# Performance work log

Measured on AMD Instinct MI355X. Metric: run time of the kernel, lower is better.

Reference implementation:

```python
import jax, jax.numpy as jnp
import numpy as np

W_DIST = 1.0
W_ANGLE = 1.0
EPS = 1e-12


def setup_inputs() -> dict:
    key = jax.random.key(0)
    k1, k2, k3 = jax.random.split(key, 3)
    B, C = 384, 512
    return {
        "feat_s": jax.random.normal(k1, (B, C), dtype=jnp.float32),
        "feat_t": jax.random.normal(k2, (B, C), dtype=jnp.float32),
        "labels": jax.random.randint(k3, (B,), 0, C, dtype=jnp.int64),
    }


def _pdist(feat):
    # Euclidean pairwise distances with zeroed diagonal (matches RKD.pdist).
    sq = jnp.sum(feat * feat, axis=1)                      # [B]
    prod = feat @ feat.T                                   # [B,B]
    d = jnp.clip(sq[None, :] + sq[:, None] - 2.0 * prod, EPS, None)
    d = jnp.sqrt(d)
    B = feat.shape[0]
    return d * (1.0 - jnp.eye(B, dtype=feat.dtype))


def _norm_pdist(feat):
    d = _pdist(feat)
    pos = d > 0
    mean_pos = jnp.sum(jnp.where(pos, d, 0.0)) / jnp.maximum(jnp.sum(pos), 1)
    return d / mean_pos


def _smooth_l1(x, y):
    a = jnp.abs(x - y)
    return jnp.mean(jnp.where(a < 1.0, 0.5 * a * a, a - 0.5))


def _angle_gram(feat):
    # vd[i, j] = feat[j] - feat[i], normalized along feature dim (F.normalize eps=1e-12)
    vd = feat[None, :, :] - feat[:, None, :]               # [B,B,C]
    nrm = jnp.sqrt(jnp.sum(vd * vd, axis=2, keepdims=True))
    vd = vd / jnp.maximum(nrm, EPS)
    return jnp.einsum('bic,bjc->bij', vd, vd)              # [B,B,B]


def _rkd(feat_s, feat_t):
    dist_loss = _smooth_l1(_norm_pdist(feat_s), _norm_pdist(feat_t))
    angle_loss = _smooth_l1(_angle_gram(feat_s), _angle_gram(feat_t))
    return W_DIST * dist_loss + W_ANGLE * angle_loss


def reference(feat_s, feat_t, labels):
    # hard CE loss (mean reduction)
    logp = jax.nn.log_softmax(feat_s, axis=-1)
    hard_loss = -jnp.mean(logp[jnp.arange(feat_s.shape[0]), labels])
    # soft RKD loss; teacher detached as in the torch code
    soft_loss = _rkd(feat_s, jax.lax.stop_gradient(feat_t))
    return hard_loss + soft_loss
```

## Files before the change

kernel.cpp:

```cpp
#include <hip/hip_runtime.h>
#include <hip/hip_bf16.h>
#include <math.h>

#define B 384
#define C 512
#define NPAIR (B * B)
#define NOFF  (B * (B - 1))

#define T16  24
#define UP16 300
#define T64  6
#define UP64 21

#define HARD_OFF 0
#define DSUM_OFF 384
#define ANG_OFF  984
#define DIST_OFF 1992
#define SQS_OFF  2016
#define SQT_OFF  2400
#define PS_OFF   2816
#define PT_OFF   (PS_OFF + NPAIR)

typedef __attribute__((ext_vector_type(8))) short short8;
typedef __attribute__((ext_vector_type(4))) float floatx4;

__device__ __forceinline__ float blk_sum(float v, float* s4, int t) {
#pragma unroll
  for (int off = 32; off > 0; off >>= 1) v += __shfl_down(v, off, 64);
  if ((t & 63) == 0) s4[t >> 6] = v;
  __syncthreads();
  float r = s4[0] + s4[1] + s4[2] + s4[3];
  __syncthreads();
  return r;
}

__device__ __forceinline__ short bfc(float x) {
  __hip_bfloat16 h = __float2bfloat16(x);
  return __builtin_bit_cast(short, h);
}

__device__ __forceinline__ short8 load_frag(const float* p) {
  float4 lo = *(const float4*)p;
  float4 hi = *(const float4*)(p + 4);
  short8 v;
  v[0] = bfc(lo.x); v[1] = bfc(lo.y); v[2] = bfc(lo.z); v[3] = bfc(lo.w);
  v[4] = bfc(hi.x); v[5] = bfc(hi.y); v[6] = bfc(hi.z); v[7] = bfc(hi.w);
  return v;
}

__global__ __launch_bounds__(256) void k_row(const float* __restrict__ fs,
                                             const float* __restrict__ ft,
                                             const int* __restrict__ lab,
                                             float* __restrict__ ws) {
  int r = blockIdx.x, t = threadIdx.x;
  const float* xs = fs + r * C;
  const float* xt = ft + r * C;
  float x0 = xs[t], x1 = xs[t + 256];
  float y0 = xt[t], y1 = xt[t + 256];
  __shared__ float s4[4];
  float m = fmaxf(x0, x1);
#pragma unroll
  for (int off = 32; off > 0; off >>= 1) m = fmaxf(m, __shfl_down(m, off, 64));
  if ((t & 63) == 0) s4[t >> 6] = m;
  __syncthreads();
  m = fmaxf(fmaxf(s4[0], s4[1]), fmaxf(s4[2], s4[3]));
  __syncthreads();
  float es = blk_sum(expf(x0 - m) + expf(x1 - m), s4, t);
  float ss = blk_sum(x0 * x0 + x1 * x1, s4, t);
  float st = blk_sum(y0 * y0 + y1 * y1, s4, t);
  if (t == 0) {
    ws[SQS_OFF + r] = ss;
    ws[SQT_OFF + r] = st;
    ws[HARD_OFF + r] = m + logf(es) - xs[lab[r]];
  }
}

__global__ __launch_bounds__(256, 4) void k_gram(const float* __restrict__ fs,
                                                 const float* __restrict__ ft,
                                                 float* __restrict__ ws) {
  int t = threadIdx.x;
  int w = t >> 6, lane = t & 63;
  int g = blockIdx.x * 4 + w;
  int tensor = (g >= UP16) ? 1 : 0;
  int uu = g - tensor * UP16;
  int ti = 0;
  while (uu >= T16 - ti) { uu -= T16 - ti; ++ti; }
  int tj = ti + uu;
  const float* F = tensor ? ft : fs;
  const float* sq = ws + (tensor ? SQT_OFF : SQS_OFF);
  float* P = ws + (tensor ? PT_OFF : PS_OFF);
  int i0 = ti * 16, j0 = tj * 16;
  int r = lane & 15, q = lane >> 4;
  const float* arow = F + (i0 + r) * C + q * 8;
  const float* brow = F + (j0 + r) * C + q * 8;
  floatx4 acc = {0.f, 0.f, 0.f, 0.f};
#pragma unroll
  for (int ks = 0; ks < 16; ++ks) {
    short8 a = load_frag(arow + ks * 32);
    short8 b = load_frag(brow + ks * 32);
    acc = __builtin_amdgcn_mfma_f32_16x16x32_bf16(a, b, acc, 0, 0, 0);
  }
  int col = lane & 15;
  int j = j0 + col;
  float sqj = sq[j];
  float dsum = 0.f;
#pragma unroll
  for (int reg = 0; reg < 4; ++reg) {
    int i = i0 + q * 4 + reg;
    float p = acc[reg];
    P[i * B + j] = p;
    P[j * B + i] = p;
    float d2 = sq[i] + sqj - 2.f * p;
    float d = sqrtf(fmaxf(d2, 1e-12f));
    float wgt = (ti < tj) ? 2.f : ((i < j) ? 2.f : 0.f);
    dsum = fmaf(wgt, d, dsum);
  }
#pragma unroll
  for (int off = 32; off > 0; off >>= 1) dsum += __shfl_down(dsum, off, 64);
  if (lane == 0) ws[DSUM_OFF + g] = dsum;
}

#define BCH 8
#define ANGLE_BODY(MASKED)                                                   \
  for (int b = 0; b < BCH; ++b) {                                            \
    float uis[4], qis[4], uit[4], qit[4], ujs[4], qjs[4], ujt[4], qjt[4];    \
    float4 v;                                                                \
    v = *(const float4*)&sI[b][0][ty * 4];                                   \
    uis[0] = v.x; uis[1] = v.y; uis[2] = v.z; uis[3] = v.w;                  \
    v = *(const float4*)&sI[b][1][ty * 4];                                   \
    qis[0] = v.x; qis[1] = v.y; qis[2] = v.z; qis[3] = v.w;                  \
    v = *(const float4*)&sI[b][2][ty * 4];                                   \
    uit[0] = v.x; uit[1] = v.y; uit[2] = v.z; uit[3] = v.w;                  \
    v = *(const float4*)&sI[b][3][ty * 4];                                   \
    qit[0] = v.x; qit[1] = v.y; qit[2] = v.z; qit[3] = v.w;                  \
    v = *(const float4*)&sJ[b][0][tx * 4];                                   \
    ujs[0] = v.x; ujs[1] = v.y; ujs[2] = v.z; ujs[3] = v.w;                  \
    v = *(const float4*)&sJ[b][1][tx * 4];                                   \
    qjs[0] = v.x; qjs[1] = v.y; qjs[2] = v.z; qjs[3] = v.w;                  \
    v = *(const float4*)&sJ[b][2][tx * 4];                                   \
    ujt[0] = v.x; ujt[1] = v.y; ujt[2] = v.z; ujt[3] = v.w;                  \
    v = *(const float4*)&sJ[b][3][tx * 4];                                   \
    qjt[0] = v.x; qjt[1] = v.y; qjt[2] = v.z; qjt[3] = v.w;                  \
    _Pragma("unroll")                                                        \
    for (int r = 0; r < 4; ++r) {                                            \
      _Pragma("unroll")                                                      \
      for (int c = 0; c < 4; ++c) {                                          \
        float f1s = fmaf(uis[r], ps[r][c], -qis[r]);                         \
        float gs = fmaf(ujs[c], f1s, -(uis[r] * qjs[c]));                    \
        float f1t = fmaf(uit[r], pt[r][c], -qit[r]);                         \
        float gt = fmaf(ujt[c], f1t, -(uit[r] * qjt[c]));                    \
        float a = fabsf(gs - gt);                                            \
        if (MASKED) a = (ty * 4 + r < tx * 4 + c) ? a : 0.f;                 \
        float mm = fminf(a, 1.f);                                            \
        acc = fmaf(mm, fmaf(-0.5f, mm, a), acc);                             \
      }                                                                      \
    }                                                                        \
  }

__global__ __launch_bounds__(256, 4) void k_angle(float* __restrict__ ws) {
  const float* Ps = ws + PS_OFF;
  const float* Pt = ws + PT_OFF;
  const float* sqs = ws + SQS_OFF;
  const float* sqt = ws + SQT_OFF;
  int uu = blockIdx.x;
  int ti = 0;
  while (uu >= T64 - ti) { uu -= T64 - ti; ++ti; }
  int tj = ti + uu;
  int i0 = ti * 64, j0 = tj * 64;
  bool diag = (ti == tj);
  int b0 = blockIdx.y * BCH;
  int t = threadIdx.x;
  int ty = t >> 4, tx = t & 15;

  __shared__ float sI[BCH][4][64];
  __shared__ float sJ[BCH][4][64];
  __shared__ float s4[4];

  float ps[4][4], pt[4][4];
#pragma unroll
  for (int r = 0; r < 4; ++r) {
    float4 v = *(const float4*)&Ps[(i0 + ty * 4 + r) * B + j0 + tx * 4];
    ps[r][0] = v.x; ps[r][1] = v.y; ps[r][2] = v.z; ps[r][3] = v.w;
    v = *(const float4*)&Pt[(i0 + ty * 4 + r) * B + j0 + tx * 4];
    pt[r][0] = v.x; pt[r][1] = v.y; pt[r][2] = v.z; pt[r][3] = v.w;
  }

  for (int idx = t; idx < BCH * 128; idx += 256) {
    int b = idx >> 7, p = idx & 127;
    int bb = b0 + b;
    int col = (p < 64) ? (i0 + p) : (j0 + p - 64);
    float pvs = Ps[bb * B + col];
    float pvt = Pt[bb * B + col];
    float pbbs = Ps[bb * B + bb];
    float pbbt = Pt[bb * B + bb];
    float d2s = sqs[bb] + sqs[col] - 2.f * pvs;
    float d2t = sqt[bb] + sqt[col] - 2.f * pvt;
    float us = (col == bb) ? 0.f : rsqrtf(fmaxf(d2s, 1e-24f));
    float ut = (col == bb) ? 0.f : rsqrtf(fmaxf(d2t, 1e-24f));
    float qs = us * (pvs - 0.5f * pbbs);
    float qt = ut * (pvt - 0.5f * pbbt);
    float* dst = (p < 64) ? &sI[b][0][p] : &sJ[b][0][p - 64];
    dst[0] = us; dst[64] = qs; dst[128] = ut; dst[192] = qt;
  }
  __syncthreads();

  float acc = 0.f;
  if (diag) { ANGLE_BODY(true) } else { ANGLE_BODY(false) }

  float asum = blk_sum(acc, s4, t);
  if (t == 0) ws[ANG_OFF + blockIdx.y * UP64 + blockIdx.x] = asum;

  if (blockIdx.y == 0) {
    float ssum = 0.f, tsum = 0.f;
    for (int i = t; i < UP16; i += 256) ssum += ws[DSUM_OFF + i];
    for (int i = t; i < UP16; i += 256) tsum += ws[DSUM_OFF + UP16 + i];
    ssum = blk_sum(ssum, s4, t);
    tsum = blk_sum(tsum, s4, t);
    float inv_ms = (float)NOFF / ssum;
    float inv_mt = (float)NOFF / tsum;
    float sqsi[4], sqti[4], sqsj[4], sqtj[4];
#pragma unroll
    for (int r = 0; r < 4; ++r) {
      sqsi[r] = sqs[i0 + ty * 4 + r];
      sqti[r] = sqt[i0 + ty * 4 + r];
      sqsj[r] = sqs[j0 + tx * 4 + r];
      sqtj[r] = sqt[j0 + tx * 4 + r];
    }
    float dacc = 0.f;
#pragma unroll
    for (int r = 0; r < 4; ++r)
#pragma unroll
      for (int c = 0; c < 4; ++c) {
        float d2s = sqsi[r] + sqsj[c] - 2.f * ps[r][c];
        float d2t = sqti[r] + sqtj[c] - 2.f * pt[r][c];
        float ds = sqrtf(fmaxf(d2s, 1e-12f)) * inv_ms;
        float dt = sqrtf(fmaxf(d2t, 1e-12f)) * inv_mt;
        float a = fabsf(ds - dt);
        if (diag) a = (ty * 4 + r < tx * 4 + c) ? a : 0.f;
        float mm = fminf(a, 1.f);
        dacc = fmaf(mm, fmaf(-0.5f, mm, a), dacc);
      }
    float dsum2 = blk_sum(dacc, s4, t);
    if (t == 0) ws[DIST_OFF + blockIdx.x] = dsum2;
  }
}

__global__ __launch_bounds__(256) void k_final(const float* __restrict__ ws,
                                               float* __restrict__ out) {
  __shared__ float s4[4];
  int t = threadIdx.x;
  float h = 0.f;
  for (int i = t; i < B; i += 256) h += ws[HARD_OFF + i];
  float a = 0.f;
  for (int i = t; i < UP64 * 48; i += 256) a += ws[ANG_OFF + i];
  float d = 0.f;
  for (int i = t; i < UP64; i += 256) d += ws[DIST_OFF + i];
  h = blk_sum(h, s4, t);
  a = blk_sum(a, s4, t);
  d = blk_sum(d, s4, t);
  if (t == 0)
    out[0] = h * (1.f / (float)B) + 2.f * d * (1.f / (float)NPAIR) +
             2.f * a * (1.f / 56623104.f);
}

extern "C" void kernel_launch(void* const* d_in, const int* in_sizes, int n_in,
                              void* d_out, int out_size, void* d_ws, size_t ws_size,
                              hipStream_t stream) {
  (void)in_sizes; (void)n_in; (void)out_size; (void)ws_size;
  const float* fs = (const float*)d_in[0];
  const float* ft = (const float*)d_in[1];
  const int* lab = (const int*)d_in[2];
  float* ws = (float*)d_ws;
  float* out = (float*)d_out;

  k_row<<<B, 256, 0, stream>>>(fs, ft, lab, ws);
  k_gram<<<150, 256, 0, stream>>>(fs, ft, ws);
  k_angle<<<dim3(UP64, 48), 256, 0, stream>>>(ws);
  k_final<<<1, 256, 0, stream>>>(ws, out);
}
```

Baseline: 86.67 us.

## Fuse final reduction into angle kernel via atomic ticket; one row per wave

```diff
diff --git a/kernel.cpp b/kernel.cpp
--- a/kernel.cpp
+++ b/kernel.cpp
@@ -11,6 +11,7 @@
 #define UP16 300
 #define T64  6
 #define UP64 21
+#define NANG (UP64 * 48)
 
 #define HARD_OFF 0
 #define DSUM_OFF 384
@@ -18,6 +19,7 @@
 #define DIST_OFF 1992
 #define SQS_OFF  2016
 #define SQT_OFF  2400
+#define CNT_OFF  2784
 #define PS_OFF   2816
 #define PT_OFF   (PS_OFF + NPAIR)
 
@@ -52,23 +54,33 @@
                                              const float* __restrict__ ft,
                                              const int* __restrict__ lab,
                                              float* __restrict__ ws) {
-  int r = blockIdx.x, t = threadIdx.x;
+  int t = threadIdx.x;
+  int wv = t >> 6, lane = t & 63;
+  int r = blockIdx.x * 4 + wv;
   const float* xs = fs + r * C;
   const float* xt = ft + r * C;
-  float x0 = xs[t], x1 = xs[t + 256];
-  float y0 = xt[t], y1 = xt[t + 256];
-  __shared__ float s4[4];
-  float m = fmaxf(x0, x1);
+  float4 a0 = *(const float4*)&xs[lane * 8];
+  float4 a1 = *(const float4*)&xs[lane * 8 + 4];
+  float4 b0 = *(const float4*)&xt[lane * 8];
+  float4 b1 = *(const float4*)&xt[lane * 8 + 4];
+  float m = fmaxf(fmaxf(fmaxf(a0.x, a0.y), fmaxf(a0.z, a0.w)),
+                  fmaxf(fmaxf(a1.x, a1.y), fmaxf(a1.z, a1.w)));
 #pragma unroll
   for (int off = 32; off > 0; off >>= 1) m = fmaxf(m, __shfl_down(m, off, 64));
-  if ((t & 63) == 0) s4[t >> 6] = m;
-  __syncthreads();
-  m = fmaxf(fmaxf(s4[0], s4[1]), fmaxf(s4[2], s4[3]));
-  __syncthreads();
-  float es = blk_sum(expf(x0 - m) + expf(x1 - m), s4, t);
-  float ss = blk_sum(x0 * x0 + x1 * x1, s4, t);
-  float st = blk_sum(y0 * y0 + y1 * y1, s4, t);
-  if (t == 0) {
+  m = __shfl(m, 0, 64);
+  float es = expf(a0.x - m) + expf(a0.y - m) + expf(a0.z - m) + expf(a0.w - m) +
+             expf(a1.x - m) + expf(a1.y - m) + expf(a1.z - m) + expf(a1.w - m);
+  float ss = a0.x * a0.x + a0.y * a0.y + a0.z * a0.z + a0.w * a0.w +
+             a1.x * a1.x + a1.y * a1.y + a1.z * a1.z + a1.w * a1.w;
+  float st = b0.x * b0.x + b0.y * b0.y + b0.z * b0.z + b0.w * b0.w +
+             b1.x * b1.x + b1.y * b1.y + b1.z * b1.z + b1.w * b1.w;
+#pragma unroll
+  for (int off = 32; off > 0; off >>= 1) {
+    es += __shfl_down(es, off, 64);
+    ss += __shfl_down(ss, off, 64);
+    st += __shfl_down(st, off, 64);
+  }
+  if (lane == 0) {
     ws[SQS_OFF + r] = ss;
     ws[SQT_OFF + r] = st;
     ws[HARD_OFF + r] = m + logf(es) - xs[lab[r]];
@@ -79,6 +91,7 @@
                                                  const float* __restrict__ ft,
                                                  float* __restrict__ ws) {
   int t = threadIdx.x;
+  if (blockIdx.x == 0 && t == 0) ((unsigned int*)ws)[CNT_OFF] = 0u;
   int w = t >> 6, lane = t & 63;
   int g = blockIdx.x * 4 + w;
   int tensor = (g >= UP16) ? 1 : 0;
@@ -157,7 +170,8 @@
     }                                                                        \
   }
 
-__global__ __launch_bounds__(256, 4) void k_angle(float* __restrict__ ws) {
+__global__ __launch_bounds__(256, 4) void k_angle(float* __restrict__ ws,
+                                                  float* __restrict__ out) {
   const float* Ps = ws + PS_OFF;
   const float* Pt = ws + PT_OFF;
   const float* sqs = ws + SQS_OFF;
@@ -175,6 +189,7 @@
   __shared__ float sI[BCH][4][64];
   __shared__ float sJ[BCH][4][64];
   __shared__ float s4[4];
+  __shared__ unsigned int s_ticket;
 
   float ps[4][4], pt[4][4];
 #pragma unroll
@@ -233,9 +248,9 @@
       for (int c = 0; c < 4; ++c) {
         float d2s = sqsi[r] + sqsj[c] - 2.f * ps[r][c];
         float d2t = sqti[r] + sqtj[c] - 2.f * pt[r][c];
-        float ds = sqrtf(fmaxf(d2s, 1e-12f)) * inv_ms;
-        float dt = sqrtf(fmaxf(d2t, 1e-12f)) * inv_mt;
-        float a = fabsf(ds - dt);
+        float dsv = sqrtf(fmaxf(d2s, 1e-12f)) * inv_ms;
+        float dtv = sqrtf(fmaxf(d2t, 1e-12f)) * inv_mt;
+        float a = fabsf(dsv - dtv);
         if (diag) a = (ty * 4 + r < tx * 4 + c) ? a : 0.f;
         float mm = fminf(a, 1.f);
         dacc = fmaf(mm, fmaf(-0.5f, mm, a), dacc);
@@ -243,24 +258,23 @@
     float dsum2 = blk_sum(dacc, s4, t);
     if (t == 0) ws[DIST_OFF + blockIdx.x] = dsum2;
   }
-}
-
-__global__ __launch_bounds__(256) void k_final(const float* __restrict__ ws,
-                                               float* __restrict__ out) {
-  __shared__ float s4[4];
-  int t = threadIdx.x;
-  float h = 0.f;
-  for (int i = t; i < B; i += 256) h += ws[HARD_OFF + i];
-  float a = 0.f;
-  for (int i = t; i < UP64 * 48; i += 256) a += ws[ANG_OFF + i];
-  float d = 0.f;
-  for (int i = t; i < UP64; i += 256) d += ws[DIST_OFF + i];
-  h = blk_sum(h, s4, t);
-  a = blk_sum(a, s4, t);
-  d = blk_sum(d, s4, t);
-  if (t == 0)
-    out[0] = h * (1.f / (float)B) + 2.f * d * (1.f / (float)NPAIR) +
-             2.f * a * (1.f / 56623104.f);
+
+  __threadfence();
+  if (t == 0) s_ticket = atomicAdd((unsigned int*)ws + CNT_OFF, 1u);
+  __syncthreads();
+  if (s_ticket == NANG - 1) {
+    __threadfence();
+    float h = 0.f, aa = 0.f, dd = 0.f;
+    for (int i = t; i < B; i += 256) h += ws[HARD_OFF + i];
+    for (int i = t; i < NANG; i += 256) aa += ws[ANG_OFF + i];
+    for (int i = t; i < UP64; i += 256) dd += ws[DIST_OFF + i];
+    h = blk_sum(h, s4, t);
+    aa = blk_sum(aa, s4, t);
+    dd = blk_sum(dd, s4, t);
+    if (t == 0)
+      out[0] = h * (1.f / (float)B) + 2.f * dd * (1.f / (float)NPAIR) +
+               2.f * aa * (1.f / 56623104.f);
+  }
 }
 
 extern "C" void kernel_launch(void* const* d_in, const int* in_sizes, int n_in,
@@ -273,8 +287,7 @@
   float* ws = (float*)d_ws;
   float* out = (float*)d_out;
 
-  k_row<<<B, 256, 0, stream>>>(fs, ft, lab, ws);
+  k_row<<<96, 256, 0, stream>>>(fs, ft, lab, ws);
   k_gram<<<150, 256, 0, stream>>>(fs, ft, ws);
-  k_angle<<<dim3(UP64, 48), 256, 0, stream>>>(ws);
-  k_final<<<1, 256, 0, stream>>>(ws, out);
-}
+  k_angle<<<dim3(UP64, 48), 256, 0, stream>>>(ws, out);
+}
```

Result: slower. 138.8 us (+60.2%).
